# Performance work log

Measured on AMD Instinct MI355X. Metric: run time of the kernel, lower is better.

The kernel has to match this reference:

```python
import jax, jax.numpy as jnp
import numpy as np
from jax import lax

EPS = 1e-5

def _layernorm(x, g, b):
    m = jnp.mean(x, axis=-1, keepdims=True)
    v = jnp.mean((x - m) ** 2, axis=-1, keepdims=True)
    return (x - m) * lax.rsqrt(v + EPS) * g + b

def _dwconv(x, H, W, w, b):
    # x: [B, N, C], w: [C, 1, 3, 3] (OIHW, depthwise), b: [C]
    B, N, C = x.shape
    xi = x.transpose(0, 2, 1).reshape(B, C, H, W)
    y = lax.conv_general_dilated(
        xi, w, window_strides=(1, 1), padding='SAME',
        feature_group_count=C,
        dimension_numbers=('NCHW', 'OIHW', 'NCHW'))
    y = y + b[None, :, None, None]
    return y.reshape(B, C, H * W).transpose(0, 2, 1)

def _channel_attn(x, groups, qkv_w, qkv_b, proj_w, proj_b):
    B, N, C = x.shape
    hd = C // groups
    qkv = x @ qkv_w.T + qkv_b                       # [B, N, 3C]
    qkv = qkv.reshape(B, N, 3, groups, hd)
    q, k, v = qkv[:, :, 0], qkv[:, :, 1], qkv[:, :, 2]   # [B, N, g, hd]
    q = q * (float(N) ** -0.5)
    attn = jnp.einsum('bngc,bngd->bgcd', q, k)      # [B, g, hd, hd]
    attn = jax.nn.softmax(attn, axis=-1)
    out = jnp.einsum('bgcd,bngd->bngc', attn, v)    # [B, N, g, hd]
    out = out.reshape(B, N, C)
    return out @ proj_w.T + proj_b

def _block(x, H, W, dw1_w, dw1_b, ln1_g, ln1_b, qkv_w, qkv_b, proj_w, proj_b,
           dw2_w, dw2_b, ln2_g, ln2_b, fc1_w, fc1_b, fc2_w, fc2_b, groups=8):
    # conv1 (no norm) + residual
    x = x + _dwconv(x, H, W, dw1_w, dw1_b)
    # prenorm channel attention + residual
    x = x + _channel_attn(_layernorm(x, ln1_g, ln1_b), groups, qkv_w, qkv_b, proj_w, proj_b)
    # conv2 (no norm) + residual
    x = x + _dwconv(x, H, W, dw2_w, dw2_b)
    # prenorm MLP + residual
    h = _layernorm(x, ln2_g, ln2_b)
    h = jax.nn.gelu(h @ fc1_w.T + fc1_b, approximate=False)
    x = x + (h @ fc2_w.T + fc2_b)
    return x

def setup_inputs() -> dict:
    key = jax.random.key(0)
    B, H, W, C, groups, ratio = 32, 32, 32, 768, 8, 4
    N, Ch = H * W, C * ratio
    ks = jax.random.split(key, 16)
    s = lambda fan: 1.0 / np.sqrt(fan)
    return {
        'x': jax.random.normal(ks[0], (B, N, C), jnp.float32),
        'H': H, 'W': W,
        'dw1_w': jax.random.normal(ks[1], (C, 1, 3, 3), jnp.float32) * s(9),
        'dw1_b': jnp.zeros((C,), jnp.float32),
        'ln1_g': jnp.ones((C,), jnp.float32),
        'ln1_b': jnp.zeros((C,), jnp.float32),
        'qkv_w': jax.random.normal(ks[2], (3 * C, C), jnp.float32) * s(C),
        'qkv_b': jnp.zeros((3 * C,), jnp.float32),
        'proj_w': jax.random.normal(ks[3], (C, C), jnp.float32) * s(C),
        'proj_b': jnp.zeros((C,), jnp.float32),
        'dw2_w': jax.random.normal(ks[4], (C, 1, 3, 3), jnp.float32) * s(9),
        'dw2_b': jnp.zeros((C,), jnp.float32),
        'ln2_g': jnp.ones((C,), jnp.float32),
        'ln2_b': jnp.zeros((C,), jnp.float32),
        'fc1_w': jax.random.normal(ks[5], (Ch, C), jnp.float32) * s(C),
        'fc1_b': jnp.zeros((Ch,), jnp.float32),
        'fc2_w': jax.random.normal(ks[6], (C, Ch), jnp.float32) * s(Ch),
        'fc2_b': jnp.zeros((C,), jnp.float32),
    }

def reference(x, H, W, dw1_w, dw1_b, ln1_g, ln1_b, qkv_w, qkv_b, proj_w, proj_b,
              dw2_w, dw2_b, ln2_g, ln2_b, fc1_w, fc1_b, fc2_w, fc2_b):
    return _block(x, H, W, dw1_w, dw1_b, ln1_g, ln1_b, qkv_w, qkv_b, proj_w, proj_b,
                  dw2_w, dw2_b, ln2_g, ln2_b, fc1_w, fc1_b, fc2_w, fc2_b)
```

## Files before the change

### kernel.cpp

```cpp
#include <hip/hip_runtime.h>

typedef unsigned short ushort_t;
typedef __bf16 v8bf __attribute__((ext_vector_type(8)));
typedef float v4f __attribute__((ext_vector_type(4)));

#define B_ 32
#define N_ 1024
#define C_ 768
#define G_ 8
#define HD_ 96
#define CH_ 3072
#define M_ 32768

static __device__ __forceinline__ float b2f(ushort_t u) {
    union { float f; unsigned int i; } z; z.i = ((unsigned int)u) << 16; return z.f;
}
static __device__ __forceinline__ ushort_t f2b(float f) {
    unsigned int u = __float_as_uint(f);
    u += 0x7fff + ((u >> 16) & 1);
    return (ushort_t)(u >> 16);
}
static __device__ __forceinline__ unsigned int pk2(float a, float b) {
    return (unsigned int)f2b(a) | ((unsigned int)f2b(b) << 16);
}

#define GLOAD_LDS16(g, l) __builtin_amdgcn_global_load_lds( \
    (const __attribute__((address_space(1))) unsigned int*)(g), \
    (__attribute__((address_space(3))) unsigned int*)(l), 16, 0, 0)

__global__ __launch_bounds__(256) void cvt_bf16(
    const float* __restrict__ in, ushort_t* __restrict__ out)
{
    int i = (blockIdx.x * 256 + threadIdx.x) * 4;
    float4 v = *(const float4*)(in + i);
    uint2 p; p.x = pk2(v.x, v.y); p.y = pk2(v.z, v.w);
    *(uint2*)(out + i) = p;
}

__global__ __launch_bounds__(256) void transpose_w(
    const float* __restrict__ w, float* __restrict__ wt)
{
    int i = blockIdx.x * 256 + threadIdx.x;
    int c = i / 9, k = i % 9;
    wt[k * C_ + c] = w[i];
}

__global__ __launch_bounds__(256) void dwconv_add(
    const float* __restrict__ xin, const float* __restrict__ wt,
    const float* __restrict__ bias, float* __restrict__ out)
{
    int t = threadIdx.x;
    int bid = blockIdx.x;
    int cblk = bid % 6;
    int bh = bid / 6;
    int b = bh >> 5, h = bh & 31;
    int tw = t >> 5;
    int c0 = cblk * 128 + (t & 31) * 4;
    int w0 = tw * 4;

    float4 tap[3][6];
#pragma unroll
    for (int dh = 0; dh < 3; dh++) {
        int hh = h + dh - 1;
        bool hok = (hh >= 0) && (hh < 32);
#pragma unroll
        for (int dw = 0; dw < 6; dw++) {
            int ww = w0 + dw - 1;
            bool ok = hok && (ww >= 0) && (ww < 32);
            if (ok)
                tap[dh][dw] = *(const float4*)(
                    xin + (size_t)((b << 10) | (hh << 5) | ww) * C_ + c0);
            else
                tap[dh][dw] = make_float4(0.f, 0.f, 0.f, 0.f);
        }
    }
    float4 wv[9];
#pragma unroll
    for (int k = 0; k < 9; k++)
        wv[k] = *(const float4*)(wt + k * C_ + c0);
    float4 bv = *(const float4*)(bias + c0);

#pragma unroll
    for (int i = 0; i < 4; i++) {
        float4 acc = bv;
#pragma unroll
        for (int dh = 0; dh < 3; dh++)
#pragma unroll
            for (int dw = 0; dw < 3; dw++) {
                float4 xv = tap[dh][i + dw];
                float4 wk = wv[dh * 3 + dw];
                acc.x += wk.x * xv.x; acc.y += wk.y * xv.y;
                acc.z += wk.z * xv.z; acc.w += wk.w * xv.w;
            }
        float4 xr = tap[1][i + 1];
        acc.x += xr.x; acc.y += xr.y; acc.z += xr.z; acc.w += xr.w;
        *(float4*)(out + (size_t)((b << 10) | (h << 5) | (w0 + i)) * C_ + c0) = acc;
    }
}

__global__ __launch_bounds__(256) void layernorm_bf(
    const float* __restrict__ xin, const float* __restrict__ g,
    const float* __restrict__ bb, ushort_t* __restrict__ out)
{
    int row = blockIdx.x;
    int t = threadIdx.x;
    const float* xr = xin + (size_t)row * C_;
    float x0 = xr[t], x1 = xr[t + 256], x2 = xr[t + 512];
    float s1 = x0 + x1 + x2;
    float s2 = x0 * x0 + x1 * x1 + x2 * x2;
#pragma unroll
    for (int o = 32; o > 0; o >>= 1) {
        s1 += __shfl_xor(s1, o);
        s2 += __shfl_xor(s2, o);
    }
    __shared__ float red[8];
    if ((t & 63) == 0) { red[(t >> 6) * 2] = s1; red[(t >> 6) * 2 + 1] = s2; }
    __syncthreads();
    s1 = red[0] + red[2] + red[4] + red[6];
    s2 = red[1] + red[3] + red[5] + red[7];
    float m = s1 * (1.0f / 768.0f);
    float var = s2 * (1.0f / 768.0f) - m * m;
    float inv = rsqrtf(var + 1e-5f);
    ushort_t* orow = out + (size_t)row * C_;
    orow[t]       = f2b((x0 - m) * inv * g[t]       + bb[t]);
    orow[t + 256] = f2b((x1 - m) * inv * g[t + 256] + bb[t + 256]);
    orow[t + 512] = f2b((x2 - m) * inv * g[t + 512] + bb[t + 512]);
}

template <int EPI>
__global__ __launch_bounds__(256) void gemm_bt(
    const ushort_t* __restrict__ A, const ushort_t* __restrict__ W,
    const float* __restrict__ bias, const float* __restrict__ resid,
    void* __restrict__ outv, int M, int Nf, int K)
{
    __shared__ __align__(16) ushort_t ring[3][2][128 * 32];
    int t = threadIdx.x;
    int bm = blockIdx.x;
    int bn = blockIdx.y;
    int wave = t >> 6, lane = t & 63;
    int wm = (wave >> 1) * 64;
    int wn = (wave & 1) * 64;
    int row16 = lane & 15;
    int quad = lane >> 4;
    int qswz = (quad * 8) ^ (((row16 >> 1) & 3) * 8);

    int r0 = wave * 16 + (lane >> 2);
    int r1 = (wave + 4) * 16 + (lane >> 2);
    int c8s = ((lane & 3) ^ ((lane >> 3) & 3)) * 8;
    const ushort_t* Ag0 = A + (size_t)(bm * 128 + r0) * K + c8s;
    const ushort_t* Ag1 = A + (size_t)(bm * 128 + r1) * K + c8s;
    const ushort_t* Wg0 = W + (size_t)(bn * 128 + r0) * K + c8s;
    const ushort_t* Wg1 = W + (size_t)(bn * 128 + r1) * K + c8s;

    v4f acc[4][4];
#pragma unroll
    for (int i = 0; i < 4; i++)
#pragma unroll
        for (int j = 0; j < 4; j++) acc[i][j] = (v4f){0.f, 0.f, 0.f, 0.f};

    const int NT = K >> 5;

    auto STAGE = [&](int kt) {
        int s = kt % 3;
        ushort_t* a = &ring[s][0][0];
        ushort_t* b = &ring[s][1][0];
        int off = kt * 32;
        GLOAD_LDS16(Ag0 + off, a + wave * 512);
        GLOAD_LDS16(Ag1 + off, a + (wave + 4) * 512);
        GLOAD_LDS16(Wg0 + off, b + wave * 512);
        GLOAD_LDS16(Wg1 + off, b + (wave + 4) * 512);
    };

    STAGE(0);
    STAGE(1);
    asm volatile("s_waitcnt vmcnt(4)" ::: "memory");
    __builtin_amdgcn_s_barrier();

    for (int kt = 0; kt < NT; ++kt) {
        if (kt + 2 < NT) STAGE(kt + 2);

        const ushort_t* sA = &ring[kt % 3][0][0];
        const ushort_t* sB = &ring[kt % 3][1][0];
        v8bf af[4], bfr[4];
#pragma unroll
        for (int i = 0; i < 4; i++)
            af[i] = *(const v8bf*)(sA + (wm + i * 16 + row16) * 32 + qswz);
#pragma unroll
        for (int j = 0; j < 4; j++)
            bfr[j] = *(const v8bf*)(sB + (wn + j * 16 + row16) * 32 + qswz);
#pragma unroll
        for (int i = 0; i < 4; i++)
#pragma unroll
            for (int j = 0; j < 4; j++)
                acc[i][j] = __builtin_amdgcn_mfma_f32_16x16x32_bf16(af[i], bfr[j], acc[i][j], 0, 0, 0);

        if (kt + 1 < NT) {
            if (kt + 2 < NT)
                asm volatile("s_waitcnt vmcnt(4)" ::: "memory");
            else
                asm volatile("s_waitcnt vmcnt(0)" ::: "memory");
            __builtin_amdgcn_s_barrier();
        }
    }

#pragma unroll
    for (int i = 0; i < 4; i++) {
#pragma unroll
        for (int j = 0; j < 4; j++) {
            int col = bn * 128 + wn + j * 16 + row16;
            float bv = bias[col];
#pragma unroll
            for (int r = 0; r < 4; r++) {
                int row = bm * 128 + wm + i * 16 + quad * 4 + r;
                float v = acc[i][j][r] + bv;
                if (EPI == 1) v = 0.5f * v * (1.0f + erff(v * 0.70710678118f));
                if (EPI == 2) {
                    v += resid[(size_t)row * Nf + col];
                    ((float*)outv)[(size_t)row * Nf + col] = v;
                } else {
                    ((ushort_t*)outv)[(size_t)row * Nf + col] = f2b(v);
                }
            }
        }
    }
}

__global__ __launch_bounds__(256) void chan_attn(
    const ushort_t* __restrict__ qkv, ushort_t* __restrict__ P)
{
    __shared__ __align__(16) char smem[96 * 97 * 4];
    ushort_t* sQt = (ushort_t*)smem;
    ushort_t* sKt = (ushort_t*)(smem + 96 * 72 * 2);
    float* sS = (float*)smem;
    int bg = blockIdx.x;
    int b = bg >> 3, g = bg & 7;
    int t = threadIdx.x;
    int wave = t >> 6, lane = t & 63;
    int wc = (wave >> 1) * 48, wd = (wave & 1) * 48;
    int row16 = lane & 15, quad = lane >> 4;

    v4f acc[3][3];
#pragma unroll
    for (int i = 0; i < 3; i++)
#pragma unroll
        for (int j = 0; j < 3; j++) acc[i][j] = (v4f){0.f, 0.f, 0.f, 0.f};

    for (int n0 = 0; n0 < N_; n0 += 64) {
        __syncthreads();
#pragma unroll
        for (int i = 0; i < 3; i++) {
            int li = t * 3 + i;
            int r = li / 12, sg = li % 12;
            size_t qoff = ((size_t)(b * N_ + n0 + r) * 3) * C_ + g * HD_ + sg * 8;
            union { uint4 v; ushort_t s[8]; } uq, uk;
            uq.v = *(const uint4*)(qkv + qoff);
            uk.v = *(const uint4*)(qkv + qoff + C_);
#pragma unroll
            for (int k = 0; k < 8; k++) {
                sQt[(sg * 8 + k) * 72 + r] = uq.s[k];
                sKt[(sg * 8 + k) * 72 + r] = uk.s[k];
            }
        }
        __syncthreads();
#pragma unroll
        for (int kk = 0; kk < 64; kk += 32) {
            v8bf af[3], bfr[3];
#pragma unroll
            for (int i = 0; i < 3; i++)
                af[i] = *(const v8bf*)(sQt + (wc + i * 16 + row16) * 72 + kk + quad * 8);
#pragma unroll
            for (int j = 0; j < 3; j++)
                bfr[j] = *(const v8bf*)(sKt + (wd + j * 16 + row16) * 72 + kk + quad * 8);
#pragma unroll
            for (int i = 0; i < 3; i++)
#pragma unroll
                for (int j = 0; j < 3; j++)
                    acc[i][j] = __builtin_amdgcn_mfma_f32_16x16x32_bf16(af[i], bfr[j], acc[i][j], 0, 0, 0);
        }
    }
    __syncthreads();
#pragma unroll
    for (int i = 0; i < 3; i++)
#pragma unroll
        for (int j = 0; j < 3; j++)
#pragma unroll
            for (int r = 0; r < 4; r++) {
                int c = wc + i * 16 + quad * 4 + r;
                int d = wd + j * 16 + row16;
                sS[c * 97 + d] = acc[i][j][r] * 0.03125f;
            }
    __syncthreads();
    if (t < 96) {
        float mx = -1e30f;
        for (int d = 0; d < 96; d++) mx = fmaxf(mx, sS[t * 97 + d]);
        float sum = 0.f;
        for (int d = 0; d < 96; d++) sum += __expf(sS[t * 97 + d] - mx);
        float rs = 1.0f / sum;
        ushort_t* prow = P + (size_t)bg * 9216 + t * 96;
        for (int d = 0; d < 96; d++) prow[d] = f2b(__expf(sS[t * 97 + d] - mx) * rs);
    }
}

__global__ __launch_bounds__(256) void attn_av(
    const ushort_t* __restrict__ qkv, const ushort_t* __restrict__ P,
    ushort_t* __restrict__ out)
{
    __shared__ __align__(16) ushort_t sV[256 * 104];
    __shared__ __align__(16) ushort_t sP[96 * 104];
    int blk = blockIdx.x;
    int nch = blk & 3, g = (blk >> 2) & 7, b = blk >> 5;
    int t = threadIdx.x;
    int n0 = nch * 256;
#pragma unroll
    for (int i = 0; i < 12; i++) {
        int li = t + i * 256;
        int r = li / 12, sg = li % 12;
        size_t voff = ((size_t)(b * N_ + n0 + r) * 3 + 2) * C_ + g * HD_ + sg * 8;
        *(uint4*)(sV + r * 104 + sg * 8) = *(const uint4*)(qkv + voff);
    }
#pragma unroll
    for (int i = 0; i < 5; i++) {
        int li = t + i * 256;
        if (li < 1152) {
            int r = li / 12, sg = li % 12;
            *(uint4*)(sP + r * 104 + sg * 8) =
                *(const uint4*)(P + (size_t)(b * 8 + g) * 9216 + li * 8);
        }
    }
    __syncthreads();
    int wave = t >> 6, lane = t & 63;
    int wm = wave * 64;
    int row16 = lane & 15, quad = lane >> 4;
    v4f acc[4][6];
#pragma unroll
    for (int i = 0; i < 4; i++)
#pragma unroll
        for (int j = 0; j < 6; j++) acc[i][j] = (v4f){0.f, 0.f, 0.f, 0.f};
#pragma unroll
    for (int kk = 0; kk < 96; kk += 32) {
        v8bf af[4], bfr[6];
#pragma unroll
        for (int i = 0; i < 4; i++)
            af[i] = *(const v8bf*)(sV + (wm + i * 16 + row16) * 104 + kk + quad * 8);
#pragma unroll
        for (int j = 0; j < 6; j++)
            bfr[j] = *(const v8bf*)(sP + (j * 16 + row16) * 104 + kk + quad * 8);
#pragma unroll
        for (int i = 0; i < 4; i++)
#pragma unroll
            for (int j = 0; j < 6; j++)
                acc[i][j] = __builtin_amdgcn_mfma_f32_16x16x32_bf16(af[i], bfr[j], acc[i][j], 0, 0, 0);
    }
#pragma unroll
    for (int i = 0; i < 4; i++)
#pragma unroll
        for (int j = 0; j < 6; j++)
#pragma unroll
            for (int r = 0; r < 4; r++) {
                int n = n0 + wm + i * 16 + quad * 4 + r;
                int c = j * 16 + row16;
                out[(size_t)(b * N_ + n) * C_ + g * HD_ + c] = f2b(acc[i][j][r]);
            }
}

extern "C" void kernel_launch(void* const* d_in, const int* in_sizes, int n_in,
                              void* d_out, int out_size, void* d_ws, size_t ws_size,
                              hipStream_t stream)
{
    const float* x      = (const float*)d_in[0];
    const float* dw1_w  = (const float*)d_in[3];
    const float* dw1_b  = (const float*)d_in[4];
    const float* ln1_g  = (const float*)d_in[5];
    const float* ln1_b  = (const float*)d_in[6];
    const float* qkv_w  = (const float*)d_in[7];
    const float* qkv_b  = (const float*)d_in[8];
    const float* proj_w = (const float*)d_in[9];
    const float* proj_b = (const float*)d_in[10];
    const float* dw2_w  = (const float*)d_in[11];
    const float* dw2_b  = (const float*)d_in[12];
    const float* ln2_g  = (const float*)d_in[13];
    const float* ln2_b  = (const float*)d_in[14];
    const float* fc1_w  = (const float*)d_in[15];
    const float* fc1_b  = (const float*)d_in[16];
    const float* fc2_w  = (const float*)d_in[17];
    const float* fc2_b  = (const float*)d_in[18];
    float* outp = (float*)d_out;

    char* ws = (char*)d_ws;
    ushort_t* qkvW = (ushort_t*)ws;
    ushort_t* projW = qkvW + 2304 * 768;
    ushort_t* fc1W = projW + 768 * 768;
    ushort_t* fc2W = fc1W + 3072 * 768;
    const size_t WB = (size_t)(2304*768 + 768*768 + 3072*768 + 768*3072) * 2;
    float* wt1 = (float*)(ws + WB);
    float* wt2 = wt1 + 9 * C_;
    const size_t WTB = 2 * 9 * C_ * sizeof(float);

    size_t CB = 32;
    while (CB > 1 && WB + WTB + CB * 12730368ull > ws_size) CB >>= 1;
    const size_t R = CB * 1024;
    char* act = ws + WB + WTB;
    ushort_t* L  = (ushort_t*)act;
    ushort_t* Ab = (ushort_t*)(act + R * C_ * 2);
    float*    X2 = (float*)(act + 2 * R * C_ * 2);
    ushort_t* P  = (ushort_t*)(act + 2 * R * C_ * 2 + R * C_ * 4);
    ushort_t* D  = (ushort_t*)(act + 2 * R * C_ * 2 + R * C_ * 4 + CB * 147456);

    cvt_bf16<<<2304 * 768 / 1024, 256, 0, stream>>>(qkv_w, qkvW);
    cvt_bf16<<<768 * 768 / 1024, 256, 0, stream>>>(proj_w, projW);
    cvt_bf16<<<3072 * 768 / 1024, 256, 0, stream>>>(fc1_w, fc1W);
    cvt_bf16<<<768 * 3072 / 1024, 256, 0, stream>>>(fc2_w, fc2W);
    transpose_w<<<27, 256, 0, stream>>>(dw1_w, wt1);
    transpose_w<<<27, 256, 0, stream>>>(dw2_w, wt2);

    dwconv_add<<<32 * 32 * 6, 256, 0, stream>>>(x, wt1, dw1_b, outp);

    const int nchunk = (int)(32 / CB);
    for (int c = 0; c < nchunk; c++) {
        float* xc = outp + (size_t)c * R * C_;
        layernorm_bf<<<(int)R, 256, 0, stream>>>(xc, ln1_g, ln1_b, L);
        gemm_bt<0><<<dim3((int)R / 128, 2304 / 128), 256, 0, stream>>>(
            L, qkvW, qkv_b, nullptr, D, (int)R, 2304, C_);
        chan_attn<<<(int)CB * 8, 256, 0, stream>>>(D, P);
        attn_av<<<(int)CB * 32, 256, 0, stream>>>(D, P, Ab);
        gemm_bt<2><<<dim3((int)R / 128, C_ / 128), 256, 0, stream>>>(
            Ab, projW, proj_b, xc, X2, (int)R, C_, C_);
        dwconv_add<<<(int)(R / 1024) * 32 * 6, 256, 0, stream>>>(X2, wt2, dw2_b, xc);
        layernorm_bf<<<(int)R, 256, 0, stream>>>(xc, ln2_g, ln2_b, L);
        gemm_bt<1><<<dim3((int)R / 128, CH_ / 128), 256, 0, stream>>>(
            L, fc1W, fc1_b, nullptr, D, (int)R, CH_, C_);
        gemm_bt<2><<<dim3((int)R / 128, C_ / 128), 256, 0, stream>>>(
            D, fc2W, fc2_b, xc, xc, (int)R, C_, CH_);
    }
}
```

Measured before the change: 1.181 ms.

## Merge weight prep launches, compute two rows per dwconv thread, prefetch QK tiles

Folds the four bf16 weight conversions into one launch and the two depthwise-weight transposes into another, which cuts launch overhead. The depthwise conv now computes two output rows per thread from a 4-row tap window, so overlapping input rows are loaded fewer times, at the cost of more registers. The channel-attention kernel loads the next Q/K tile into registers while the current tile's MFMAs run, hiding global load latency but raising register pressure.

```diff
diff --git a/kernel.cpp b/kernel.cpp
--- a/kernel.cpp
+++ b/kernel.cpp
@@ -28,19 +28,31 @@
     (const __attribute__((address_space(1))) unsigned int*)(g), \
     (__attribute__((address_space(3))) unsigned int*)(l), 16, 0, 0)
 
-__global__ __launch_bounds__(256) void cvt_bf16(
-    const float* __restrict__ in, ushort_t* __restrict__ out)
-{
-    int i = (blockIdx.x * 256 + threadIdx.x) * 4;
-    float4 v = *(const float4*)(in + i);
+__global__ __launch_bounds__(256) void cvt_all(
+    const float* __restrict__ a, const float* __restrict__ b,
+    const float* __restrict__ c, const float* __restrict__ d,
+    ushort_t* __restrict__ o)
+{
+    int blk = blockIdx.x;
+    const float* src; ushort_t* dst; int off;
+    if (blk < 1728)      { src = a; dst = o;                          off = blk; }
+    else if (blk < 2304) { src = b; dst = o + 2304 * 768;             off = blk - 1728; }
+    else if (blk < 4608) { src = c; dst = o + 2304 * 768 + 768 * 768; off = blk - 2304; }
+    else                 { src = d; dst = o + 2304 * 768 + 768 * 768 + 3072 * 768; off = blk - 4608; }
+    int i = (off * 256 + threadIdx.x) * 4;
+    float4 v = *(const float4*)(src + i);
     uint2 p; p.x = pk2(v.x, v.y); p.y = pk2(v.z, v.w);
-    *(uint2*)(out + i) = p;
-}
-
-__global__ __launch_bounds__(256) void transpose_w(
-    const float* __restrict__ w, float* __restrict__ wt)
-{
-    int i = blockIdx.x * 256 + threadIdx.x;
+    *(uint2*)(dst + i) = p;
+}
+
+__global__ __launch_bounds__(256) void transpose_w2(
+    const float* __restrict__ w1, const float* __restrict__ w2,
+    float* __restrict__ wt1, float* __restrict__ wt2)
+{
+    int blk = blockIdx.x;
+    const float* w = (blk < 27) ? w1 : w2;
+    float* wt = (blk < 27) ? wt1 : wt2;
+    int i = (blk % 27) * 256 + threadIdx.x;
     int c = i / 9, k = i % 9;
     wt[k * C_ + c] = w[i];
 }
@@ -52,16 +64,17 @@
     int t = threadIdx.x;
     int bid = blockIdx.x;
     int cblk = bid % 6;
-    int bh = bid / 6;
-    int b = bh >> 5, h = bh & 31;
+    int bhp = bid / 6;
+    int b = bhp >> 4, hp = bhp & 15;
+    int h0 = hp * 2;
     int tw = t >> 5;
     int c0 = cblk * 128 + (t & 31) * 4;
     int w0 = tw * 4;
 
-    float4 tap[3][6];
-#pragma unroll
-    for (int dh = 0; dh < 3; dh++) {
-        int hh = h + dh - 1;
+    float4 tap[4][6];
+#pragma unroll
+    for (int dh = 0; dh < 4; dh++) {
+        int hh = h0 + dh - 1;
         bool hok = (hh >= 0) && (hh < 32);
 #pragma unroll
         for (int dw = 0; dw < 6; dw++) {
@@ -81,20 +94,23 @@
     float4 bv = *(const float4*)(bias + c0);
 
 #pragma unroll
-    for (int i = 0; i < 4; i++) {
-        float4 acc = bv;
-#pragma unroll
-        for (int dh = 0; dh < 3; dh++)
-#pragma unroll
-            for (int dw = 0; dw < 3; dw++) {
-                float4 xv = tap[dh][i + dw];
-                float4 wk = wv[dh * 3 + dw];
-                acc.x += wk.x * xv.x; acc.y += wk.y * xv.y;
-                acc.z += wk.z * xv.z; acc.w += wk.w * xv.w;
-            }
-        float4 xr = tap[1][i + 1];
-        acc.x += xr.x; acc.y += xr.y; acc.z += xr.z; acc.w += xr.w;
-        *(float4*)(out + (size_t)((b << 10) | (h << 5) | (w0 + i)) * C_ + c0) = acc;
+    for (int row = 0; row < 2; row++) {
+#pragma unroll
+        for (int i = 0; i < 4; i++) {
+            float4 acc = bv;
+#pragma unroll
+            for (int dh = 0; dh < 3; dh++)
+#pragma unroll
+                for (int dw = 0; dw < 3; dw++) {
+                    float4 xv = tap[row + dh][i + dw];
+                    float4 wk = wv[dh * 3 + dw];
+                    acc.x += wk.x * xv.x; acc.y += wk.y * xv.y;
+                    acc.z += wk.z * xv.z; acc.w += wk.w * xv.w;
+                }
+            float4 xr = tap[row + 1][i + 1];
+            acc.x += xr.x; acc.y += xr.y; acc.z += xr.z; acc.w += xr.w;
+            *(float4*)(out + (size_t)((b << 10) | ((h0 + row) << 5) | (w0 + i)) * C_ + c0) = acc;
+        }
     }
 }
 
@@ -230,7 +246,7 @@
 {
     __shared__ __align__(16) char smem[96 * 97 * 4];
     ushort_t* sQt = (ushort_t*)smem;
-    ushort_t* sKt = (ushort_t*)(smem + 96 * 72 * 2);
+    ushort_t* sKt = (ushort_t*)(smem + 13824);
     float* sS = (float*)smem;
     int bg = blockIdx.x;
     int b = bg >> 3, g = bg & 7;
@@ -239,43 +255,66 @@
     int wc = (wave >> 1) * 48, wd = (wave & 1) * 48;
     int row16 = lane & 15, quad = lane >> 4;
 
+    int li0 = t * 3;
+    int r_[3], sg_[3];
+#pragma unroll
+    for (int i = 0; i < 3; i++) { r_[i] = (li0 + i) / 12; sg_[i] = (li0 + i) % 12; }
+
     v4f acc[3][3];
 #pragma unroll
     for (int i = 0; i < 3; i++)
 #pragma unroll
         for (int j = 0; j < 3; j++) acc[i][j] = (v4f){0.f, 0.f, 0.f, 0.f};
 
+    uint4 uq[3], uk[3];
+#pragma unroll
+    for (int i = 0; i < 3; i++) {
+        const ushort_t* p = qkv + ((size_t)(b * N_ + r_[i]) * 3) * C_ + g * HD_ + sg_[i] * 8;
+        uq[i] = *(const uint4*)p;
+        uk[i] = *(const uint4*)(p + C_);
+    }
+
     for (int n0 = 0; n0 < N_; n0 += 64) {
+        uint4 nq[3] = {}, nk[3] = {};
+        bool more = (n0 + 64 < N_);
+        if (more) {
+#pragma unroll
+            for (int i = 0; i < 3; i++) {
+                const ushort_t* p = qkv + ((size_t)(b * N_ + n0 + 64 + r_[i]) * 3) * C_ + g * HD_ + sg_[i] * 8;
+                nq[i] = *(const uint4*)p;
+                nk[i] = *(const uint4*)(p + C_);
+            }
+        }
         __syncthreads();
 #pragma unroll
         for (int i = 0; i < 3; i++) {
-            int li = t * 3 + i;
-            int r = li / 12, sg = li % 12;
-            size_t qoff = ((size_t)(b * N_ + n0 + r) * 3) * C_ + g * HD_ + sg * 8;
-            union { uint4 v; ushort_t s[8]; } uq, uk;
-            uq.v = *(const uint4*)(qkv + qoff);
-            uk.v = *(const uint4*)(qkv + qoff + C_);
-#pragma unroll
-            for (int k = 0; k < 8; k++) {
-                sQt[(sg * 8 + k) * 72 + r] = uq.s[k];
-                sKt[(sg * 8 + k) * 72 + r] = uk.s[k];
+            union { uint4 v; ushort_t s[8]; } a, bu;
+            a.v = uq[i]; bu.v = uk[i];
+#pragma unroll
+            for (int k2 = 0; k2 < 8; k2++) {
+                sQt[(sg_[i] * 8 + k2) * 72 + r_[i]] = a.s[k2];
+                sKt[(sg_[i] * 8 + k2) * 72 + r_[i]] = bu.s[k2];
             }
         }
         __syncthreads();
 #pragma unroll
         for (int kk = 0; kk < 64; kk += 32) {
-            v8bf af[3], bfr[3];
+            v8bf af[3], bf2[3];
 #pragma unroll
             for (int i = 0; i < 3; i++)
                 af[i] = *(const v8bf*)(sQt + (wc + i * 16 + row16) * 72 + kk + quad * 8);
 #pragma unroll
             for (int j = 0; j < 3; j++)
-                bfr[j] = *(const v8bf*)(sKt + (wd + j * 16 + row16) * 72 + kk + quad * 8);
+                bf2[j] = *(const v8bf*)(sKt + (wd + j * 16 + row16) * 72 + kk + quad * 8);
 #pragma unroll
             for (int i = 0; i < 3; i++)
 #pragma unroll
                 for (int j = 0; j < 3; j++)
-                    acc[i][j] = __builtin_amdgcn_mfma_f32_16x16x32_bf16(af[i], bfr[j], acc[i][j], 0, 0, 0);
+                    acc[i][j] = __builtin_amdgcn_mfma_f32_16x16x32_bf16(af[i], bf2[j], acc[i][j], 0, 0, 0);
+        }
+        if (more) {
+#pragma unroll
+            for (int i = 0; i < 3; i++) { uq[i] = nq[i]; uk[i] = nk[i]; }
         }
     }
     __syncthreads();
@@ -406,14 +445,10 @@
     ushort_t* P  = (ushort_t*)(act + 2 * R * C_ * 2 + R * C_ * 4);
     ushort_t* D  = (ushort_t*)(act + 2 * R * C_ * 2 + R * C_ * 4 + CB * 147456);
 
-    cvt_bf16<<<2304 * 768 / 1024, 256, 0, stream>>>(qkv_w, qkvW);
-    cvt_bf16<<<768 * 768 / 1024, 256, 0, stream>>>(proj_w, projW);
-    cvt_bf16<<<3072 * 768 / 1024, 256, 0, stream>>>(fc1_w, fc1W);
-    cvt_bf16<<<768 * 3072 / 1024, 256, 0, stream>>>(fc2_w, fc2W);
-    transpose_w<<<27, 256, 0, stream>>>(dw1_w, wt1);
-    transpose_w<<<27, 256, 0, stream>>>(dw2_w, wt2);
-
-    dwconv_add<<<32 * 32 * 6, 256, 0, stream>>>(x, wt1, dw1_b, outp);
+    cvt_all<<<6912, 256, 0, stream>>>(qkv_w, proj_w, fc1_w, fc2_w, qkvW);
+    transpose_w2<<<54, 256, 0, stream>>>(dw1_w, dw2_w, wt1, wt2);
+
+    dwconv_add<<<32 * 16 * 6, 256, 0, stream>>>(x, wt1, dw1_b, outp);
 
     const int nchunk = (int)(32 / CB);
     for (int c = 0; c < nchunk; c++) {
@@ -425,7 +460,7 @@
         attn_av<<<(int)CB * 32, 256, 0, stream>>>(D, P, Ab);
         gemm_bt<2><<<dim3((int)R / 128, C_ / 128), 256, 0, stream>>>(
             Ab, projW, proj_b, xc, X2, (int)R, C_, C_);
-        dwconv_add<<<(int)(R / 1024) * 32 * 6, 256, 0, stream>>>(X2, wt2, dw2_b, xc);
+        dwconv_add<<<(int)(R / 1024) * 16 * 6, 256, 0, stream>>>(X2, wt2, dw2_b, xc);
         layernorm_bf<<<(int)R, 256, 0, stream>>>(xc, ln2_g, ln2_b, L);
         gemm_bt<1><<<dim3((int)R / 128, CH_ / 128), 256, 0, stream>>>(
             L, fc1W, fc1_b, nullptr, D, (int)R, CH_, C_);
```

Measured after the change: 1.153 ms. -2.4%, faster.
